# Kernel tuning notes

Hardware: AMD Instinct MI355X
Metric: run time of the kernel (lower is better)

Reference implementation:

```python
import jax, jax.numpy as jnp
import numpy as np

N, D = 1024, 64  # n_nodes, inputSize == hiddenSize == cellSize


def setup_inputs() -> dict:
    key = jax.random.key(0)
    ks = jax.random.split(key, 9)
    inputs = jax.random.normal(ks[0], (N, D), dtype=jnp.float32)
    # sparse-ish binary adjacency, no self loops
    adj = (jax.random.uniform(ks[1], (N, N)) < 0.03).astype(jnp.float32)
    adj = adj.at[jnp.arange(N), jnp.arange(N)].set(0.0)
    numNei = jnp.maximum(adj.sum(axis=1), 1.0)  # avoid div-by-zero
    # initStates() in torch uses randn for h0/c0
    h0 = jax.random.normal(ks[2], (N, D), dtype=jnp.float32)
    c0 = jax.random.normal(ks[3], (N, D), dtype=jnp.float32)
    # torch nn.Linear default init: U(-1/sqrt(fan_in), 1/sqrt(fan_in))
    s_g = 1.0 / np.sqrt(2 * D)
    s_h = 1.0 / np.sqrt(D)
    Wg = jax.random.uniform(ks[4], (D, 2 * D), minval=-s_g, maxval=s_g, dtype=jnp.float32)
    bg = jax.random.uniform(ks[5], (D,), minval=-s_g, maxval=s_g, dtype=jnp.float32)
    Ws = jax.random.uniform(ks[6], (D, D), minval=-s_h, maxval=s_h, dtype=jnp.float32)
    bs = jax.random.uniform(ks[7], (D,), minval=-s_h, maxval=s_h, dtype=jnp.float32)
    Wn = jax.random.uniform(ks[8], (D, D), minval=-s_h, maxval=s_h, dtype=jnp.float32)
    sequence = jnp.arange(N, dtype=jnp.int32)
    return {"inputs": inputs, "neighbour": adj, "numNei": numNei,
            "h0": h0, "c0": c0, "Wg": Wg, "bg": bg, "Ws": Ws, "bs": bs,
            "Wn": Wn, "sequence": sequence}


def reference(inputs, neighbour, numNei, h0, c0, Wg, bg, Ws, bs, Wn, sequence):
    def step(carry, idx):
        H, C = carry                       # [N, D] each
        inp = inputs[idx]                  # [D]
        h_i = H[idx]                       # [D]
        c_i = C[idx]                       # [D] (torch passes cellState[index])
        nei = neighbour[idx]               # [N] adjacency row
        num = numNei[idx]
        # neighbour-averaged hidden state
        neiH = (nei @ H) / num             # [D]
        pre = jnp.concatenate([inp, h_i]) @ Wg.T + bg + neiH @ Wn.T  # [D]
        inputState = jax.nn.sigmoid(pre)
        outputState = inputState           # identical expression in torch
        helpCell = jnp.tanh(pre)
        fs = inp @ Ws.T + bs               # selfGate(inp), [D]
        # forgetSelfMat broadcast of fs over all nodes
        neiForget = jax.nn.sigmoid(fs[None, :] + H @ Wn.T)   # [N, D]
        forgetState = jax.nn.sigmoid(fs + h_i @ Wn.T)        # [D]
        c_new = (nei @ (neiForget * c_i[None, :])) / num \
                + forgetState * c_i + inputState * helpCell  # [D]
        h_new = jnp.tanh(outputState * c_new)
        return (H.at[idx].set(h_new), C.at[idx].set(c_new)), None

    (Hf, _Cf), _ = jax.lax.scan(step, (h0, c0), sequence)
    # torch: residualHidden aliases hiddenState and is mutated in-place,
    # so `hiddenState + residualHidden` == 2 * final hidden state.
    return Hf + Hf
```

## Files before the change

kernel.cpp:

```cpp
#include <hip/hip_runtime.h>

#define NN 1024
#define DD 64
#define CAP 96
#define RCAP 128
#define SENT 32768
#define NL2E -1.44269504088896f

typedef __attribute__((ext_vector_type(8))) short bf16x8;
typedef __attribute__((ext_vector_type(4))) float f32x4;

__device__ uint4    WnFragD[8*64];
__device__ float    FSd[NN*DD];
__device__ float    Gd[NN*DD];
__device__ float    preBaseD[NN*DD];
__device__ float    fpreD[NN*DD];
__device__ float4   nodeDatD[NN*DD];
__device__ int      lowNeiD[NN*CAP + 64];
__device__ int      revNeiD[NN*RCAP];
__device__ int      revCntD[NN];
__device__ int2     hdrD[NN];
__device__ int      posArr[NN];
__device__ float    invNumD[NN];

__device__ __forceinline__ float sigm(float x)  { return 1.0f / (1.0f + __expf(-x)); }
__device__ __forceinline__ float tanhf_(float x){ return 2.0f / (1.0f + __expf(-2.0f*x)) - 1.0f; }
__device__ __forceinline__ unsigned short bf16r(float x) {
  unsigned u = __float_as_uint(x);
  u = u + 0x7fffu + ((u >> 16) & 1u);
  return (unsigned short)(u >> 16);
}

__global__ __launch_bounds__(256) void k_node(const int* __restrict__ seq,
                                              const float* __restrict__ numNei,
                                              const float* __restrict__ inputs,
                                              const float* __restrict__ h0,
                                              const float* __restrict__ Wg,
                                              const float* __restrict__ bg,
                                              const float* __restrict__ Ws,
                                              const float* __restrict__ bs,
                                              const float* __restrict__ Wn) {
  __shared__ float x_l[4][64];
  __shared__ float hh_l[4][64];
  int tid = threadIdx.x;
  int gid = blockIdx.x * 256 + tid;
  if (gid < NN) { posArr[seq[gid]] = gid; invNumD[gid] = 1.0f / numNei[gid]; revCntD[gid] = 0; }
  if (gid < 512) {
    int st = gid >> 6, lane = gid & 63;
    int s = st >> 2, t = st & 3;
    int row = 16*t + (lane & 15);
    int k0 = 32*s + 8*(lane >> 4);
    const float* wr = &Wn[row*64 + k0];
    uint4 f;
    f.x = (unsigned)bf16r(wr[0]) | ((unsigned)bf16r(wr[1]) << 16);
    f.y = (unsigned)bf16r(wr[2]) | ((unsigned)bf16r(wr[3]) << 16);
    f.z = (unsigned)bf16r(wr[4]) | ((unsigned)bf16r(wr[5]) << 16);
    f.w = (unsigned)bf16r(wr[6]) | ((unsigned)bf16r(wr[7]) << 16);
    WnFragD[st*64 + lane] = f;
  }
  for (int e2 = gid; e2 < NN*CAP; e2 += 256*256) lowNeiD[e2] = SENT;
  int w = tid >> 6, d = tid & 63;
  int i = blockIdx.x * 4 + w;
  x_l[w][d]  = inputs[i*DD + d];
  hh_l[w][d] = h0[i*DD + d];
  __syncthreads();
  float afs = bs[d], apre = bg[d], ag0 = 0.0f;
  const float4* wsr = (const float4*)&Ws[d*64];
  const float4* wnr = (const float4*)&Wn[d*64];
  const float4* wga = (const float4*)&Wg[d*128];
  const float4* wgb = (const float4*)&Wg[d*128 + 64];
  #pragma unroll 4
  for (int k4 = 0; k4 < 16; ++k4) {
    float4 ws4 = wsr[k4], wn4 = wnr[k4], wa4 = wga[k4], wb4 = wgb[k4];
    const float* wsp = (const float*)&ws4;
    const float* wnp = (const float*)&wn4;
    const float* wap = (const float*)&wa4;
    const float* wbp = (const float*)&wb4;
    #pragma unroll
    for (int j = 0; j < 4; ++j) {
      int k = 4*k4 + j;
      float xk = x_l[w][k], hk = hh_l[w][k];
      afs  += xk * wsp[j];
      ag0  += hk * wnp[j];
      apre += xk * wap[j] + hk * wbp[j];
    }
  }
  FSd[i*DD + d]      = afs;
  Gd[i*DD + d]       = ag0;
  preBaseD[i*DD + d] = apre;
  fpreD[i*DD + d]    = sigm(afs + ag0);
}

__global__ __launch_bounds__(256) void k_edges(const float* __restrict__ adj,
                                               const float* __restrict__ c0) {
  int tid = threadIdx.x;
  int w = tid >> 6, d = tid & 63;
  int i = blockIdx.x * 4 + w;
  int pi = posArr[i];
  float fs = FSd[i*DD + d];
  float accP = 0.0f, accS = 0.0f;
  int cnt = 0;
  for (int base = 0; base < NN; base += 64) {
    float a = adj[i*NN + base + d];
    unsigned long long mask = __ballot(a != 0.0f);
    while (mask) {
      int b = __ffsll(mask) - 1;
      mask &= (mask - 1);
      int j = base + b;
      if (posArr[j] < pi) {
        if (d == 0 && cnt < 64) {
          lowNeiD[i*CAP + cnt] = j << 5;
          int slot = atomicAdd(&revCntD[j], 1);
          if (slot < RCAP) revNeiD[j*RCAP + slot] = i;
        }
        cnt++;
      } else {
        float g = Gd[j*DD + d];
        accP += g;
        accS += sigm(fs + g);
      }
    }
  }
  float inv = invNumD[i];
  if (d == 0) {
    int ccap = (cnt < 64) ? cnt : 64;
    hdrD[i] = make_int2(ccap, __float_as_int(inv));
  }
  float c0v = c0[i*DD + d];
  float civ = c0v * inv;
  nodeDatD[i*DD + d] = make_float4(NL2E * fs,
                                   preBaseD[i*DD + d] + accP * inv,
                                   civ,
                                   c0v * fpreD[i*DD + d] + civ * accS);
}

__global__ __launch_bounds__(1024, 4) void k_seq(float* __restrict__ out) {
  __shared__ unsigned long long Gl64[(NN*DD + 64)/4];
  __shared__ unsigned low8p[NN][4];
  __shared__ int      queue_[NN];
  __shared__ int      indeg[NN];
  __shared__ float    invL[NN];
  __shared__ unsigned short hstage[16][64];
  __shared__ int head, tail;
  unsigned short* Gl = (unsigned short*)Gl64;
  int tid  = threadIdx.x;
  int lane = tid & 63, w = tid >> 6;
  if (tid == 0) { head = 0; tail = 0; }
  queue_[tid] = -1;
  int2 hdr = hdrD[tid];
  int  rc  = revCntD[tid];
  int  cnt0 = hdr.x;
  indeg[tid] = cnt0 | (cnt0 << 8) | (rc << 15);
  invL[tid]  = __int_as_float(hdr.y);
  {
    uint4 a = *(const uint4*)&lowNeiD[tid*CAP];
    uint4 b = *(const uint4*)&lowNeiD[tid*CAP + 4];
    low8p[tid][0] = (a.x & 0xffffu) | (a.y << 16);
    low8p[tid][1] = (a.z & 0xffffu) | (a.w << 16);
    low8p[tid][2] = (b.x & 0xffffu) | (b.y << 16);
    low8p[tid][3] = (b.z & 0xffffu) | (b.w << 16);
  }
  if (tid < 16) Gl64[NN*DD/4 + tid] = 0ull;
  uint4 fb[2][4];
  #pragma unroll
  for (int s = 0; s < 2; ++s) {
    #pragma unroll
    for (int t = 0; t < 4; ++t)
      fb[s][t] = WnFragD[(s*4 + t)*64 + lane];
  }
  __syncthreads();
  if (cnt0 == 0) {
    int p = __hip_atomic_fetch_add(&tail, 1, __ATOMIC_RELAXED, __HIP_MEMORY_SCOPE_WORKGROUP);
    __hip_atomic_store(&queue_[p], tid | (rc << 17), __ATOMIC_RELEASE, __HIP_MEMORY_SCOPE_WORKGROUP);
  }
  __syncthreads();

  int t0 = 0;
  if (lane == 0) t0 = __hip_atomic_fetch_add(&head, 1, __ATOMIC_RELAXED, __HIP_MEMORY_SCOPE_WORKGROUP);
  int t = __builtin_amdgcn_readfirstlane(t0);
  int e = -1;
  if (t < NN) {
    e = __hip_atomic_load(&queue_[t], __ATOMIC_ACQUIRE, __HIP_MEMORY_SCOPE_WORKGROUP);
    while (e < 0)
      e = __hip_atomic_load(&queue_[t], __ATOMIC_ACQUIRE, __HIP_MEMORY_SCOPE_WORKGROUP);
  } else {
    return;
  }
  e = __builtin_amdgcn_readfirstlane(e);

  int    i, cnt, rcnt, jb2v, r0, r1;
  float4 nd;
  float  inv;
  uint4  lvv;
  #define ISSUE(E) do {                                               \
    i    = (E) & 1023;                                                \
    cnt  = ((E) >> 10) & 127;                                         \
    rcnt = ((E) >> 17) & 255;                                         \
    nd   = nodeDatD[i*DD + lane];                                     \
    jb2v = lowNeiD[i*CAP + 8 + lane];                                 \
    r0   = (lane < rcnt)      ? revNeiD[i*RCAP + lane]      : -1;     \
    r1   = (lane + 64 < rcnt) ? revNeiD[i*RCAP + 64 + lane] : -1;     \
    inv  = invL[i];                                                   \
    lvv  = *(uint4*)&low8p[i][0];                                     \
  } while (0)
  ISSUE(e);

  float4 tA0 = {0,0,0,0}, tA1 = {0,0,0,0};
  int    tB0 = 0, tB1 = 0;

  for (;;) {
    asm volatile("" :: "v"(tA0.x), "v"(tA0.y), "v"(tA0.z), "v"(tA0.w),
                       "v"(tA1.x), "v"(tA1.y), "v"(tA1.z), "v"(tA1.w),
                       "v"(tB0), "v"(tB1));
    float fs2n = nd.x;
    float accG = 0.0f, accS = 0.0f;
    float g0[8], g1[8], g2[8], g3[8];
    #define LD(c) __uint_as_float(((unsigned)Gl[((c) << 1) + lane]) << 16)
    if (cnt > 0) {
      unsigned v0=lvv.x&0xffffu, v1=lvv.x>>16, v2=lvv.y&0xffffu, v3=lvv.y>>16;
      unsigned v4=lvv.z&0xffffu, v5=lvv.z>>16, v6=lvv.w&0xffffu, v7=lvv.w>>16;
      g0[0]=LD(v0); g0[1]=LD(v1); g0[2]=LD(v2); g0[3]=LD(v3);
      g0[4]=LD(v4); g0[5]=LD(v5); g0[6]=LD(v6); g0[7]=LD(v7);
    }
    if (cnt > 8) {
      #pragma unroll
      for (int q = 0; q < 8; ++q) g1[q] = LD(__builtin_amdgcn_readlane(jb2v, q));
    }
    if (cnt > 16) {
      #pragma unroll
      for (int q = 0; q < 8; ++q) g2[q] = LD(__builtin_amdgcn_readlane(jb2v, 8 + q));
    }
    if (cnt > 24) {
      #pragma unroll
      for (int q = 0; q < 8; ++q) g3[q] = LD(__builtin_amdgcn_readlane(jb2v, 16 + q));
    }
    auto domath = [&](float G) {
      float x_ = __builtin_fmaf(G, NL2E, fs2n);
      float e_ = __builtin_amdgcn_exp2f(x_);
      accS += __builtin_amdgcn_rcpf(1.0f + e_);
      accG += G;
    };
    if (cnt > 0) {
      #pragma unroll
      for (int q = 0; q < 8; ++q) domath(g0[q]);
    }
    if (cnt > 8) {
      #pragma unroll
      for (int q = 0; q < 8; ++q) domath(g1[q]);
    }
    if (cnt > 16) {
      #pragma unroll
      for (int q = 0; q < 8; ++q) domath(g2[q]);
    }
    if (cnt > 24) {
      #pragma unroll
      for (int q = 0; q < 8; ++q) domath(g3[q]);
    }
    if (cnt > 32) {
      for (int base = 32; base < cnt; base += 8) {
        float gg[8];
        #pragma unroll
        for (int q = 0; q < 8; ++q) gg[q] = LD(__builtin_amdgcn_readlane(jb2v, base - 8 + q));
        #pragma unroll
        for (int q = 0; q < 8; ++q) domath(gg[q]);
      }
    }
    {
      int nb8 = (cnt + 7) & ~7;
      float sig0 = __builtin_amdgcn_rcpf(1.0f + __builtin_amdgcn_exp2f(fs2n));
      accS -= (float)(nb8 - cnt) * sig0;
    }
    float pre = nd.y + inv * accG;
    float is  = sigm(pre);
    float hcl = tanhf_(pre);
    float c   = nd.z * accS + nd.w + is * hcl;
    float h   = tanhf_(is * c);
    int ic = i, r0c = r0, r1c = r1;
    if (lane == 0) t0 = __hip_atomic_fetch_add(&head, 1, __ATOMIC_RELAXED, __HIP_MEMORY_SCOPE_WORKGROUP);
    t = __builtin_amdgcn_readfirstlane(t0);
    bool done = (t >= NN);
    int e2 = -1;
    if (!done) e2 = __hip_atomic_load(&queue_[t], __ATOMIC_ACQUIRE, __HIP_MEMORY_SCOPE_WORKGROUP);
    e2 = __builtin_amdgcn_readfirstlane(e2);
    bool pre_ok = (e2 >= 0);
    if (pre_ok) ISSUE(e2);
    hstage[w][lane] = bf16r(h);
    const uint4* hv = (const uint4*)&hstage[w][0];
    uint4 fa0 = hv[lane >> 4];
    uint4 fa1 = hv[4 + (lane >> 4)];
    f32x4 z = {0.f, 0.f, 0.f, 0.f};
    f32x4 a0 = __builtin_amdgcn_mfma_f32_16x16x32_bf16(__builtin_bit_cast(bf16x8, fa0), __builtin_bit_cast(bf16x8, fb[0][0]), z, 0, 0, 0);
    f32x4 a1 = __builtin_amdgcn_mfma_f32_16x16x32_bf16(__builtin_bit_cast(bf16x8, fa0), __builtin_bit_cast(bf16x8, fb[0][1]), z, 0, 0, 0);
    f32x4 a2 = __builtin_amdgcn_mfma_f32_16x16x32_bf16(__builtin_bit_cast(bf16x8, fa0), __builtin_bit_cast(bf16x8, fb[0][2]), z, 0, 0, 0);
    f32x4 a3 = __builtin_amdgcn_mfma_f32_16x16x32_bf16(__builtin_bit_cast(bf16x8, fa0), __builtin_bit_cast(bf16x8, fb[0][3]), z, 0, 0, 0);
    a0 = __builtin_amdgcn_mfma_f32_16x16x32_bf16(__builtin_bit_cast(bf16x8, fa1), __builtin_bit_cast(bf16x8, fb[1][0]), a0, 0, 0, 0);
    a1 = __builtin_amdgcn_mfma_f32_16x16x32_bf16(__builtin_bit_cast(bf16x8, fa1), __builtin_bit_cast(bf16x8, fb[1][1]), a1, 0, 0, 0);
    a2 = __builtin_amdgcn_mfma_f32_16x16x32_bf16(__builtin_bit_cast(bf16x8, fa1), __builtin_bit_cast(bf16x8, fb[1][2]), a2, 0, 0, 0);
    a3 = __builtin_amdgcn_mfma_f32_16x16x32_bf16(__builtin_bit_cast(bf16x8, fa1), __builtin_bit_cast(bf16x8, fb[1][3]), a3, 0, 0, 0);
    float r01 = (lane & 16) ? a1[0] : a0[0];
    float r23 = (lane & 16) ? a3[0] : a2[0];
    float rg  = (lane & 32) ? r23 : r01;
    Gl[(ic << 6) + lane] = bf16r(rg);
    int push0 = -1, push1 = -1;
    if (r0c >= 0) {
      int old = __hip_atomic_fetch_add(&indeg[r0c], -1, __ATOMIC_ACQ_REL, __HIP_MEMORY_SCOPE_WORKGROUP);
      if ((old & 0xff) == 1) {
        int p = __hip_atomic_fetch_add(&tail, 1, __ATOMIC_RELAXED, __HIP_MEMORY_SCOPE_WORKGROUP);
        int en = r0c | (((old >> 8) & 127) << 10) | (((old >> 15) & 255) << 17);
        __hip_atomic_store(&queue_[p], en, __ATOMIC_RELEASE, __HIP_MEMORY_SCOPE_WORKGROUP);
        push0 = r0c;
      }
    }
    if (r1c >= 0) {
      int old = __hip_atomic_fetch_add(&indeg[r1c], -1, __ATOMIC_ACQ_REL, __HIP_MEMORY_SCOPE_WORKGROUP);
      if ((old & 0xff) == 1) {
        int p = __hip_atomic_fetch_add(&tail, 1, __ATOMIC_RELAXED, __HIP_MEMORY_SCOPE_WORKGROUP);
        int en = r1c | (((old >> 8) & 127) << 10) | (((old >> 15) & 255) << 17);
        __hip_atomic_store(&queue_[p], en, __ATOMIC_RELEASE, __HIP_MEMORY_SCOPE_WORKGROUP);
        push1 = r1c;
      }
    }
    {
      unsigned long long pm0 = __ballot(push0 >= 0);
      unsigned long long pm1 = __ballot(push1 >= 0);
      int rdA = -1, rdB = -1;
      if (pm0) {
        int b = __ffsll(pm0) - 1;
        rdA = __builtin_amdgcn_readlane(push0, b);
        pm0 &= (pm0 - 1);
      }
      if (pm0) {
        int b = __ffsll(pm0) - 1;
        rdB = __builtin_amdgcn_readlane(push0, b);
      } else if (pm1) {
        int b = __ffsll(pm1) - 1;
        rdB = __builtin_amdgcn_readlane(push1, b);
      }
      if (rdA >= 0) {
        tA0 = nodeDatD[rdA*DD + lane];
        tB0 = lowNeiD[rdA*CAP + 8 + lane];
      }
      if (rdB >= 0) {
        tA1 = nodeDatD[rdB*DD + lane];
        tB1 = lowNeiD[rdB*CAP + 8 + lane];
      }
    }
    out[ic*DD + lane] = 2.0f * h;
    if (done) break;
    if (!pre_ok) {
      int e3 = __hip_atomic_load(&queue_[t], __ATOMIC_ACQUIRE, __HIP_MEMORY_SCOPE_WORKGROUP);
      while (e3 < 0)
        e3 = __hip_atomic_load(&queue_[t], __ATOMIC_ACQUIRE, __HIP_MEMORY_SCOPE_WORKGROUP);
      e3 = __builtin_amdgcn_readfirstlane(e3);
      ISSUE(e3);
    }
  }
  #undef LD
  #undef ISSUE
}

extern "C" void kernel_launch(void* const* d_in, const int* in_sizes, int n_in,
                              void* d_out, int out_size, void* d_ws, size_t ws_size,
                              hipStream_t stream) {
  const float* inputs = (const float*)d_in[0];
  const float* adj    = (const float*)d_in[1];
  const float* numNei = (const float*)d_in[2];
  const float* h0     = (const float*)d_in[3];
  const float* c0     = (const float*)d_in[4];
  const float* Wg     = (const float*)d_in[5];
  const float* bg     = (const float*)d_in[6];
  const float* Ws     = (const float*)d_in[7];
  const float* bs     = (const float*)d_in[8];
  const float* Wn     = (const float*)d_in[9];
  const int*   seq    = (const int*)d_in[10];
  float* out = (float*)d_out;

  k_node <<<256, 256, 0, stream>>>(seq, numNei, inputs, h0, Wg, bg, Ws, bs, Wn);
  k_edges<<<256, 256, 0, stream>>>(adj, c0);
  k_seq  <<<1, 1024, 0, stream>>>(out);
}
```

Before: 216.6 us.

## Switch sequential dependency gather to push-based global atomic accumulation

The sequential kernel previously gathered each node's lower-order neighbours' G values from a large bf16 shared-memory cache when processing it. Now each finished node pushes its G value and the per-target sigmoid term directly into global accumulators (accGd/accSd) for all reverse neighbours with atomicAdd, and consumers just load the accumulated sums. This removes the shared G cache and the neighbour lists, reducing LDS footprint and per-node gather work. In exchange it adds global float atomics and a vmcnt wait on the serial critical path, plus fp32 storage instead of bf16 for the accumulated G.

```diff
diff --git a/kernel.cpp b/kernel.cpp
--- a/kernel.cpp
+++ b/kernel.cpp
@@ -2,26 +2,26 @@
 
 #define NN 1024
 #define DD 64
-#define CAP 96
 #define RCAP 128
-#define SENT 32768
 #define NL2E -1.44269504088896f
 
 typedef __attribute__((ext_vector_type(8))) short bf16x8;
 typedef __attribute__((ext_vector_type(4))) float f32x4;
 
-__device__ uint4    WnFragD[8*64];
-__device__ float    FSd[NN*DD];
-__device__ float    Gd[NN*DD];
-__device__ float    preBaseD[NN*DD];
-__device__ float    fpreD[NN*DD];
-__device__ float4   nodeDatD[NN*DD];
-__device__ int      lowNeiD[NN*CAP + 64];
-__device__ int      revNeiD[NN*RCAP];
-__device__ int      revCntD[NN];
-__device__ int2     hdrD[NN];
-__device__ int      posArr[NN];
-__device__ float    invNumD[NN];
+__device__ uint4  WnFragD[8*64];
+__device__ float  FSd[NN*DD];
+__device__ float  Gd[NN*DD];
+__device__ float  preBaseD[NN*DD];
+__device__ float  fpreD[NN*DD];
+__device__ float4 nodeDatD[NN*DD];
+__device__ float  fs2nD[(NN+1)*DD];
+__device__ float  accGd[(NN+1)*DD];
+__device__ float  accSd[(NN+1)*DD];
+__device__ int    revNeiD[NN*RCAP];
+__device__ int    revCntD[NN];
+__device__ int    cntD[NN];
+__device__ int    posArr[NN];
+__device__ float  invNumD[NN];
 
 __device__ __forceinline__ float sigm(float x)  { return 1.0f / (1.0f + __expf(-x)); }
 __device__ __forceinline__ float tanhf_(float x){ return 2.0f / (1.0f + __expf(-2.0f*x)) - 1.0f; }
@@ -58,7 +58,8 @@
     f.w = (unsigned)bf16r(wr[6]) | ((unsigned)bf16r(wr[7]) << 16);
     WnFragD[st*64 + lane] = f;
   }
-  for (int e2 = gid; e2 < NN*CAP; e2 += 256*256) lowNeiD[e2] = SENT;
+  for (int e2 = gid; e2 < NN*RCAP; e2 += 256*256) revNeiD[e2] = NN;
+  if (gid < DD) { fs2nD[NN*DD + gid] = 0.0f; accGd[NN*DD + gid] = 0.0f; accSd[NN*DD + gid] = 0.0f; }
   int w = tid >> 6, d = tid & 63;
   int i = blockIdx.x * 4 + w;
   x_l[w][d]  = inputs[i*DD + d];
@@ -108,8 +109,7 @@
       mask &= (mask - 1);
       int j = base + b;
       if (posArr[j] < pi) {
-        if (d == 0 && cnt < 64) {
-          lowNeiD[i*CAP + cnt] = j << 5;
+        if (d == 0) {
           int slot = atomicAdd(&revCntD[j], 1);
           if (slot < RCAP) revNeiD[j*RCAP + slot] = i;
         }
@@ -122,45 +122,30 @@
     }
   }
   float inv = invNumD[i];
-  if (d == 0) {
-    int ccap = (cnt < 64) ? cnt : 64;
-    hdrD[i] = make_int2(ccap, __float_as_int(inv));
-  }
+  if (d == 0) cntD[i] = cnt;
   float c0v = c0[i*DD + d];
   float civ = c0v * inv;
-  nodeDatD[i*DD + d] = make_float4(NL2E * fs,
+  nodeDatD[i*DD + d] = make_float4(inv,
                                    preBaseD[i*DD + d] + accP * inv,
                                    civ,
                                    c0v * fpreD[i*DD + d] + civ * accS);
+  fs2nD[i*DD + d] = NL2E * fs;
+  accGd[i*DD + d] = 0.0f;
+  accSd[i*DD + d] = 0.0f;
 }
 
 __global__ __launch_bounds__(1024, 4) void k_seq(float* __restrict__ out) {
-  __shared__ unsigned long long Gl64[(NN*DD + 64)/4];
-  __shared__ unsigned low8p[NN][4];
-  __shared__ int      queue_[NN];
-  __shared__ int      indeg[NN];
-  __shared__ float    invL[NN];
+  __shared__ int queue_[NN];
+  __shared__ int indeg[NN];
   __shared__ unsigned short hstage[16][64];
   __shared__ int head, tail;
-  unsigned short* Gl = (unsigned short*)Gl64;
   int tid  = threadIdx.x;
   int lane = tid & 63, w = tid >> 6;
   if (tid == 0) { head = 0; tail = 0; }
   queue_[tid] = -1;
-  int2 hdr = hdrD[tid];
-  int  rc  = revCntD[tid];
-  int  cnt0 = hdr.x;
-  indeg[tid] = cnt0 | (cnt0 << 8) | (rc << 15);
-  invL[tid]  = __int_as_float(hdr.y);
-  {
-    uint4 a = *(const uint4*)&lowNeiD[tid*CAP];
-    uint4 b = *(const uint4*)&lowNeiD[tid*CAP + 4];
-    low8p[tid][0] = (a.x & 0xffffu) | (a.y << 16);
-    low8p[tid][1] = (a.z & 0xffffu) | (a.w << 16);
-    low8p[tid][2] = (b.x & 0xffffu) | (b.y << 16);
-    low8p[tid][3] = (b.z & 0xffffu) | (b.w << 16);
-  }
-  if (tid < 16) Gl64[NN*DD/4 + tid] = 0ull;
+  int cnt0 = cntD[tid];
+  int rc   = revCntD[tid]; if (rc > 255) rc = 255;
+  indeg[tid] = cnt0 | (rc << 15);
   uint4 fb[2][4];
   #pragma unroll
   for (int s = 0; s < 2; ++s) {
@@ -188,94 +173,27 @@
   }
   e = __builtin_amdgcn_readfirstlane(e);
 
-  int    i, cnt, rcnt, jb2v, r0, r1;
+  int    i, rcnt, r0v, r1v;
   float4 nd;
-  float  inv;
-  uint4  lvv;
-  #define ISSUE(E) do {                                               \
-    i    = (E) & 1023;                                                \
-    cnt  = ((E) >> 10) & 127;                                         \
-    rcnt = ((E) >> 17) & 255;                                         \
-    nd   = nodeDatD[i*DD + lane];                                     \
-    jb2v = lowNeiD[i*CAP + 8 + lane];                                 \
-    r0   = (lane < rcnt)      ? revNeiD[i*RCAP + lane]      : -1;     \
-    r1   = (lane + 64 < rcnt) ? revNeiD[i*RCAP + 64 + lane] : -1;     \
-    inv  = invL[i];                                                   \
-    lvv  = *(uint4*)&low8p[i][0];                                     \
+  float  aG, aS;
+  #define ISSUE(E) do {                                                          \
+    i    = (E) & 1023;                                                           \
+    rcnt = ((E) >> 17) & 255;                                                    \
+    nd   = nodeDatD[i*DD + lane];                                                \
+    aG   = __hip_atomic_load(&accGd[i*DD + lane], __ATOMIC_RELAXED, __HIP_MEMORY_SCOPE_AGENT); \
+    aS   = __hip_atomic_load(&accSd[i*DD + lane], __ATOMIC_RELAXED, __HIP_MEMORY_SCOPE_AGENT); \
+    r0v  = revNeiD[i*RCAP + lane];                                               \
+    r1v  = revNeiD[i*RCAP + 64 + lane];                                          \
   } while (0)
   ISSUE(e);
 
-  float4 tA0 = {0,0,0,0}, tA1 = {0,0,0,0};
-  int    tB0 = 0, tB1 = 0;
-
   for (;;) {
-    asm volatile("" :: "v"(tA0.x), "v"(tA0.y), "v"(tA0.z), "v"(tA0.w),
-                       "v"(tA1.x), "v"(tA1.y), "v"(tA1.z), "v"(tA1.w),
-                       "v"(tB0), "v"(tB1));
-    float fs2n = nd.x;
-    float accG = 0.0f, accS = 0.0f;
-    float g0[8], g1[8], g2[8], g3[8];
-    #define LD(c) __uint_as_float(((unsigned)Gl[((c) << 1) + lane]) << 16)
-    if (cnt > 0) {
-      unsigned v0=lvv.x&0xffffu, v1=lvv.x>>16, v2=lvv.y&0xffffu, v3=lvv.y>>16;
-      unsigned v4=lvv.z&0xffffu, v5=lvv.z>>16, v6=lvv.w&0xffffu, v7=lvv.w>>16;
-      g0[0]=LD(v0); g0[1]=LD(v1); g0[2]=LD(v2); g0[3]=LD(v3);
-      g0[4]=LD(v4); g0[5]=LD(v5); g0[6]=LD(v6); g0[7]=LD(v7);
-    }
-    if (cnt > 8) {
-      #pragma unroll
-      for (int q = 0; q < 8; ++q) g1[q] = LD(__builtin_amdgcn_readlane(jb2v, q));
-    }
-    if (cnt > 16) {
-      #pragma unroll
-      for (int q = 0; q < 8; ++q) g2[q] = LD(__builtin_amdgcn_readlane(jb2v, 8 + q));
-    }
-    if (cnt > 24) {
-      #pragma unroll
-      for (int q = 0; q < 8; ++q) g3[q] = LD(__builtin_amdgcn_readlane(jb2v, 16 + q));
-    }
-    auto domath = [&](float G) {
-      float x_ = __builtin_fmaf(G, NL2E, fs2n);
-      float e_ = __builtin_amdgcn_exp2f(x_);
-      accS += __builtin_amdgcn_rcpf(1.0f + e_);
-      accG += G;
-    };
-    if (cnt > 0) {
-      #pragma unroll
-      for (int q = 0; q < 8; ++q) domath(g0[q]);
-    }
-    if (cnt > 8) {
-      #pragma unroll
-      for (int q = 0; q < 8; ++q) domath(g1[q]);
-    }
-    if (cnt > 16) {
-      #pragma unroll
-      for (int q = 0; q < 8; ++q) domath(g2[q]);
-    }
-    if (cnt > 24) {
-      #pragma unroll
-      for (int q = 0; q < 8; ++q) domath(g3[q]);
-    }
-    if (cnt > 32) {
-      for (int base = 32; base < cnt; base += 8) {
-        float gg[8];
-        #pragma unroll
-        for (int q = 0; q < 8; ++q) gg[q] = LD(__builtin_amdgcn_readlane(jb2v, base - 8 + q));
-        #pragma unroll
-        for (int q = 0; q < 8; ++q) domath(gg[q]);
-      }
-    }
-    {
-      int nb8 = (cnt + 7) & ~7;
-      float sig0 = __builtin_amdgcn_rcpf(1.0f + __builtin_amdgcn_exp2f(fs2n));
-      accS -= (float)(nb8 - cnt) * sig0;
-    }
-    float pre = nd.y + inv * accG;
+    float pre = nd.y + nd.x * aG;
     float is  = sigm(pre);
     float hcl = tanhf_(pre);
-    float c   = nd.z * accS + nd.w + is * hcl;
+    float c   = nd.z * aS + nd.w + is * hcl;
     float h   = tanhf_(is * c);
-    int ic = i, r0c = r0, r1c = r1;
+    int ic = i, rcur = rcnt, rv0 = r0v, rv1 = r1v;
     if (lane == 0) t0 = __hip_atomic_fetch_add(&head, 1, __ATOMIC_RELAXED, __HIP_MEMORY_SCOPE_WORKGROUP);
     t = __builtin_amdgcn_readfirstlane(t0);
     bool done = (t >= NN);
@@ -300,49 +218,43 @@
     float r01 = (lane & 16) ? a1[0] : a0[0];
     float r23 = (lane & 16) ? a3[0] : a2[0];
     float rg  = (lane & 32) ? r23 : r01;
-    Gl[(ic << 6) + lane] = bf16r(rg);
-    int push0 = -1, push1 = -1;
-    if (r0c >= 0) {
-      int old = __hip_atomic_fetch_add(&indeg[r0c], -1, __ATOMIC_ACQ_REL, __HIP_MEMORY_SCOPE_WORKGROUP);
+    for (int base = 0; base < rcur; base += 8) {
+      int   ids[8];
+      float fsd[8];
+      #pragma unroll
+      for (int q = 0; q < 8; ++q) {
+        int idx = base + q;
+        int id  = (idx < 64) ? __builtin_amdgcn_readlane(rv0, idx)
+                             : __builtin_amdgcn_readlane(rv1, idx - 64);
+        id = (idx < rcur) ? id : NN;
+        ids[q] = id;
+        fsd[q] = fs2nD[id*DD + lane];
+      }
+      float sv[8];
+      #pragma unroll
+      for (int q = 0; q < 8; ++q) {
+        float x_ = __builtin_fmaf(rg, NL2E, fsd[q]);
+        sv[q] = __builtin_amdgcn_rcpf(1.0f + __builtin_amdgcn_exp2f(x_));
+      }
+      #pragma unroll
+      for (int q = 0; q < 8; ++q) {
+        atomicAdd(&accSd[ids[q]*DD + lane], sv[q]);
+        atomicAdd(&accGd[ids[q]*DD + lane], rg);
+      }
+    }
+    asm volatile("s_waitcnt vmcnt(0)" ::: "memory");
+    if (lane < rcur) {
+      int old = __hip_atomic_fetch_add(&indeg[rv0], -1, __ATOMIC_ACQ_REL, __HIP_MEMORY_SCOPE_WORKGROUP);
       if ((old & 0xff) == 1) {
         int p = __hip_atomic_fetch_add(&tail, 1, __ATOMIC_RELAXED, __HIP_MEMORY_SCOPE_WORKGROUP);
-        int en = r0c | (((old >> 8) & 127) << 10) | (((old >> 15) & 255) << 17);
-        __hip_atomic_store(&queue_[p], en, __ATOMIC_RELEASE, __HIP_MEMORY_SCOPE_WORKGROUP);
-        push0 = r0c;
-      }
-    }
-    if (r1c >= 0) {
-      int old = __hip_atomic_fetch_add(&indeg[r1c], -1, __ATOMIC_ACQ_REL, __HIP_MEMORY_SCOPE_WORKGROUP);
+        __hip_atomic_store(&queue_[p], rv0 | (((old >> 15) & 255) << 17), __ATOMIC_RELEASE, __HIP_MEMORY_SCOPE_WORKGROUP);
+      }
+    }
+    if (lane + 64 < rcur) {
+      int old = __hip_atomic_fetch_add(&indeg[rv1], -1, __ATOMIC_ACQ_REL, __HIP_MEMORY_SCOPE_WORKGROUP);
       if ((old & 0xff) == 1) {
         int p = __hip_atomic_fetch_add(&tail, 1, __ATOMIC_RELAXED, __HIP_MEMORY_SCOPE_WORKGROUP);
-        int en = r1c | (((old >> 8) & 127) << 10) | (((old >> 15) & 255) << 17);
-        __hip_atomic_store(&queue_[p], en, __ATOMIC_RELEASE, __HIP_MEMORY_SCOPE_WORKGROUP);
-        push1 = r1c;
-      }
-    }
-    {
-      unsigned long long pm0 = __ballot(push0 >= 0);
-      unsigned long long pm1 = __ballot(push1 >= 0);
-      int rdA = -1, rdB = -1;
-      if (pm0) {
-        int b = __ffsll(pm0) - 1;
-        rdA = __builtin_amdgcn_readlane(push0, b);
-        pm0 &= (pm0 - 1);
-      }
-      if (pm0) {
-        int b = __ffsll(pm0) - 1;
-        rdB = __builtin_amdgcn_readlane(push0, b);
-      } else if (pm1) {
-        int b = __ffsll(pm1) - 1;
-        rdB = __builtin_amdgcn_readlane(push1, b);
-      }
-      if (rdA >= 0) {
-        tA0 = nodeDatD[rdA*DD + lane];
-        tB0 = lowNeiD[rdA*CAP + 8 + lane];
-      }
-      if (rdB >= 0) {
-        tA1 = nodeDatD[rdB*DD + lane];
-        tB1 = lowNeiD[rdB*CAP + 8 + lane];
+        __hip_atomic_store(&queue_[p], rv1 | (((old >> 15) & 255) << 17), __ATOMIC_RELEASE, __HIP_MEMORY_SCOPE_WORKGROUP);
       }
     }
     out[ic*DD + lane] = 2.0f * h;
@@ -355,7 +267,6 @@
       ISSUE(e3);
     }
   }
-  #undef LD
   #undef ISSUE
 }
 
```

Result: slower. 434.3 us (+100.5%).

## Combine four sigmoids per reciprocal and drop speculative prefetch of pushed nodes

Applied to the files above, without the earlier changes.

Neighbour gathers are regrouped into chunks of four, and each chunk's four sigmoid terms are summed over a shared denominator, so one reciprocal serves four neighbours instead of one each. Exponent inputs are clamped to avoid overflow in the product of denominators. Padding correction now works at 4-slot instead of 8-slot granularity. The ballot, readlane and cache-warming loads of newly ready nodes are removed, trimming per-step overhead on the serial critical path at the risk of colder loads later.

```diff
diff --git a/kernel.cpp b/kernel.cpp
--- a/kernel.cpp
+++ b/kernel.cpp
@@ -205,70 +205,83 @@
   } while (0)
   ISSUE(e);
 
-  float4 tA0 = {0,0,0,0}, tA1 = {0,0,0,0};
-  int    tB0 = 0, tB1 = 0;
-
   for (;;) {
-    asm volatile("" :: "v"(tA0.x), "v"(tA0.y), "v"(tA0.z), "v"(tA0.w),
-                       "v"(tA1.x), "v"(tA1.y), "v"(tA1.z), "v"(tA1.w),
-                       "v"(tB0), "v"(tB1));
     float fs2n = nd.x;
     float accG = 0.0f, accS = 0.0f;
-    float g0[8], g1[8], g2[8], g3[8];
+    float g[32];
     #define LD(c) __uint_as_float(((unsigned)Gl[((c) << 1) + lane]) << 16)
     if (cnt > 0) {
-      unsigned v0=lvv.x&0xffffu, v1=lvv.x>>16, v2=lvv.y&0xffffu, v3=lvv.y>>16;
-      unsigned v4=lvv.z&0xffffu, v5=lvv.z>>16, v6=lvv.w&0xffffu, v7=lvv.w>>16;
-      g0[0]=LD(v0); g0[1]=LD(v1); g0[2]=LD(v2); g0[3]=LD(v3);
-      g0[4]=LD(v4); g0[5]=LD(v5); g0[6]=LD(v6); g0[7]=LD(v7);
+      g[0]=LD(lvv.x & 0xffffu); g[1]=LD(lvv.x >> 16);
+      g[2]=LD(lvv.y & 0xffffu); g[3]=LD(lvv.y >> 16);
+    }
+    if (cnt > 4) {
+      g[4]=LD(lvv.z & 0xffffu); g[5]=LD(lvv.z >> 16);
+      g[6]=LD(lvv.w & 0xffffu); g[7]=LD(lvv.w >> 16);
     }
     if (cnt > 8) {
       #pragma unroll
-      for (int q = 0; q < 8; ++q) g1[q] = LD(__builtin_amdgcn_readlane(jb2v, q));
+      for (int q = 0; q < 4; ++q) g[8+q]  = LD(__builtin_amdgcn_readlane(jb2v, q));
+    }
+    if (cnt > 12) {
+      #pragma unroll
+      for (int q = 0; q < 4; ++q) g[12+q] = LD(__builtin_amdgcn_readlane(jb2v, 4+q));
     }
     if (cnt > 16) {
       #pragma unroll
-      for (int q = 0; q < 8; ++q) g2[q] = LD(__builtin_amdgcn_readlane(jb2v, 8 + q));
+      for (int q = 0; q < 4; ++q) g[16+q] = LD(__builtin_amdgcn_readlane(jb2v, 8+q));
+    }
+    if (cnt > 20) {
+      #pragma unroll
+      for (int q = 0; q < 4; ++q) g[20+q] = LD(__builtin_amdgcn_readlane(jb2v, 12+q));
     }
     if (cnt > 24) {
       #pragma unroll
-      for (int q = 0; q < 8; ++q) g3[q] = LD(__builtin_amdgcn_readlane(jb2v, 16 + q));
-    }
-    auto domath = [&](float G) {
-      float x_ = __builtin_fmaf(G, NL2E, fs2n);
-      float e_ = __builtin_amdgcn_exp2f(x_);
-      accS += __builtin_amdgcn_rcpf(1.0f + e_);
-      accG += G;
+      for (int q = 0; q < 4; ++q) g[24+q] = LD(__builtin_amdgcn_readlane(jb2v, 16+q));
+    }
+    if (cnt > 28) {
+      #pragma unroll
+      for (int q = 0; q < 4; ++q) g[28+q] = LD(__builtin_amdgcn_readlane(jb2v, 20+q));
+    }
+    auto quad = [&](float ga, float gb, float gc, float gd) {
+      float xa = fminf(__builtin_fmaf(ga, NL2E, fs2n), 25.0f);
+      float xb = fminf(__builtin_fmaf(gb, NL2E, fs2n), 25.0f);
+      float xc = fminf(__builtin_fmaf(gc, NL2E, fs2n), 25.0f);
+      float xd = fminf(__builtin_fmaf(gd, NL2E, fs2n), 25.0f);
+      float ea = __builtin_amdgcn_exp2f(xa);
+      float eb = __builtin_amdgcn_exp2f(xb);
+      float ec = __builtin_amdgcn_exp2f(xc);
+      float ed = __builtin_amdgcn_exp2f(xd);
+      float s0 = ea + eb, n0 = s0 + 2.0f;
+      float d0 = __builtin_fmaf(ea, eb, s0) + 1.0f;
+      float s1 = ec + ed, n1 = s1 + 2.0f;
+      float d1 = __builtin_fmaf(ec, ed, s1) + 1.0f;
+      float Nn = __builtin_fmaf(n0, d1, n1 * d0);
+      float Dd = d0 * d1;
+      accS = __builtin_fmaf(Nn, __builtin_amdgcn_rcpf(Dd), accS);
+      accG += (ga + gb) + (gc + gd);
     };
-    if (cnt > 0) {
-      #pragma unroll
-      for (int q = 0; q < 8; ++q) domath(g0[q]);
-    }
-    if (cnt > 8) {
-      #pragma unroll
-      for (int q = 0; q < 8; ++q) domath(g1[q]);
-    }
-    if (cnt > 16) {
-      #pragma unroll
-      for (int q = 0; q < 8; ++q) domath(g2[q]);
-    }
-    if (cnt > 24) {
-      #pragma unroll
-      for (int q = 0; q < 8; ++q) domath(g3[q]);
-    }
+    if (cnt > 0)  quad(g[0],  g[1],  g[2],  g[3]);
+    if (cnt > 4)  quad(g[4],  g[5],  g[6],  g[7]);
+    if (cnt > 8)  quad(g[8],  g[9],  g[10], g[11]);
+    if (cnt > 12) quad(g[12], g[13], g[14], g[15]);
+    if (cnt > 16) quad(g[16], g[17], g[18], g[19]);
+    if (cnt > 20) quad(g[20], g[21], g[22], g[23]);
+    if (cnt > 24) quad(g[24], g[25], g[26], g[27]);
+    if (cnt > 28) quad(g[28], g[29], g[30], g[31]);
     if (cnt > 32) {
-      for (int base = 32; base < cnt; base += 8) {
-        float gg[8];
-        #pragma unroll
-        for (int q = 0; q < 8; ++q) gg[q] = LD(__builtin_amdgcn_readlane(jb2v, base - 8 + q));
-        #pragma unroll
-        for (int q = 0; q < 8; ++q) domath(gg[q]);
+      for (int base = 32; base < cnt; base += 4) {
+        float ga = LD(__builtin_amdgcn_readlane(jb2v, base - 8));
+        float gb = LD(__builtin_amdgcn_readlane(jb2v, base - 7));
+        float gc = LD(__builtin_amdgcn_readlane(jb2v, base - 6));
+        float gd = LD(__builtin_amdgcn_readlane(jb2v, base - 5));
+        quad(ga, gb, gc, gd);
       }
     }
     {
-      int nb8 = (cnt + 7) & ~7;
-      float sig0 = __builtin_amdgcn_rcpf(1.0f + __builtin_amdgcn_exp2f(fs2n));
-      accS -= (float)(nb8 - cnt) * sig0;
+      int slots = (cnt <= 32) ? ((cnt + 3) & ~3) : (32 + ((cnt - 32 + 3) & ~3));
+      float e0   = __builtin_amdgcn_exp2f(fminf(fs2n, 25.0f));
+      float sig0 = __builtin_amdgcn_rcpf(1.0f + e0);
+      accS -= (float)(slots - cnt) * sig0;
     }
     float pre = nd.y + inv * accG;
     float is  = sigm(pre);
@@ -301,14 +314,12 @@
     float r23 = (lane & 16) ? a3[0] : a2[0];
     float rg  = (lane & 32) ? r23 : r01;
     Gl[(ic << 6) + lane] = bf16r(rg);
-    int push0 = -1, push1 = -1;
     if (r0c >= 0) {
       int old = __hip_atomic_fetch_add(&indeg[r0c], -1, __ATOMIC_ACQ_REL, __HIP_MEMORY_SCOPE_WORKGROUP);
       if ((old & 0xff) == 1) {
         int p = __hip_atomic_fetch_add(&tail, 1, __ATOMIC_RELAXED, __HIP_MEMORY_SCOPE_WORKGROUP);
         int en = r0c | (((old >> 8) & 127) << 10) | (((old >> 15) & 255) << 17);
         __hip_atomic_store(&queue_[p], en, __ATOMIC_RELEASE, __HIP_MEMORY_SCOPE_WORKGROUP);
-        push0 = r0c;
       }
     }
     if (r1c >= 0) {
@@ -317,32 +328,6 @@
         int p = __hip_atomic_fetch_add(&tail, 1, __ATOMIC_RELAXED, __HIP_MEMORY_SCOPE_WORKGROUP);
         int en = r1c | (((old >> 8) & 127) << 10) | (((old >> 15) & 255) << 17);
         __hip_atomic_store(&queue_[p], en, __ATOMIC_RELEASE, __HIP_MEMORY_SCOPE_WORKGROUP);
-        push1 = r1c;
-      }
-    }
-    {
-      unsigned long long pm0 = __ballot(push0 >= 0);
-      unsigned long long pm1 = __ballot(push1 >= 0);
-      int rdA = -1, rdB = -1;
-      if (pm0) {
-        int b = __ffsll(pm0) - 1;
-        rdA = __builtin_amdgcn_readlane(push0, b);
-        pm0 &= (pm0 - 1);
-      }
-      if (pm0) {
-        int b = __ffsll(pm0) - 1;
-        rdB = __builtin_amdgcn_readlane(push0, b);
-      } else if (pm1) {
-        int b = __ffsll(pm1) - 1;
-        rdB = __builtin_amdgcn_readlane(push1, b);
-      }
-      if (rdA >= 0) {
-        tA0 = nodeDatD[rdA*DD + lane];
-        tB0 = lowNeiD[rdA*CAP + 8 + lane];
-      }
-      if (rdB >= 0) {
-        tA1 = nodeDatD[rdB*DD + lane];
-        tB1 = lowNeiD[rdB*CAP + 8 + lane];
       }
     }
     out[ic*DD + lane] = 2.0f * h;
```

After: 209.0 us. -3.5%, faster.

## Spread sequential dependency scheduling across multiple blocks with NaN-flagged global publish

Applied to the files above, without the earlier changes.

Replaces the single-workgroup dynamic topological queue in LDS with a static round-robin assignment of sequence positions to waves across 8 blocks. Each wave spins on global memory, where unpublished G rows are marked with a NaN sentinel, until all lower-ordered neighbour G values are available, then publishes its own G row with agent-scope atomics. This drops the reverse-neighbour lists, in-degree counters and queue bookkeeping, and spreads work over more CUs. In exchange, neighbour reads go through L2 instead of LDS, G is kept in fp32 instead of bf16, and waves busy-poll, so a static ordering can stall behind slow predecessors.

```diff
diff --git a/kernel.cpp b/kernel.cpp
--- a/kernel.cpp
+++ b/kernel.cpp
@@ -3,9 +3,10 @@
 #define NN 1024
 #define DD 64
 #define CAP 96
-#define RCAP 128
 #define SENT 32768
 #define NL2E -1.44269504088896f
+#define NBLK 8
+#define NWAVE (NBLK*16)
 
 typedef __attribute__((ext_vector_type(8))) short bf16x8;
 typedef __attribute__((ext_vector_type(4))) float f32x4;
@@ -16,9 +17,8 @@
 __device__ float    preBaseD[NN*DD];
 __device__ float    fpreD[NN*DD];
 __device__ float4   nodeDatD[NN*DD];
+__device__ float    GpubD[(NN+1)*DD];
 __device__ int      lowNeiD[NN*CAP + 64];
-__device__ int      revNeiD[NN*RCAP];
-__device__ int      revCntD[NN];
 __device__ int2     hdrD[NN];
 __device__ int      posArr[NN];
 __device__ float    invNumD[NN];
@@ -44,7 +44,7 @@
   __shared__ float hh_l[4][64];
   int tid = threadIdx.x;
   int gid = blockIdx.x * 256 + tid;
-  if (gid < NN) { posArr[seq[gid]] = gid; invNumD[gid] = 1.0f / numNei[gid]; revCntD[gid] = 0; }
+  if (gid < NN) { posArr[seq[gid]] = gid; invNumD[gid] = 1.0f / numNei[gid]; }
   if (gid < 512) {
     int st = gid >> 6, lane = gid & 63;
     int s = st >> 2, t = st & 3;
@@ -58,6 +58,7 @@
     f.w = (unsigned)bf16r(wr[6]) | ((unsigned)bf16r(wr[7]) << 16);
     WnFragD[st*64 + lane] = f;
   }
+  if (gid < DD) GpubD[NN*DD + gid] = 0.0f;
   for (int e2 = gid; e2 < NN*CAP; e2 += 256*256) lowNeiD[e2] = SENT;
   int w = tid >> 6, d = tid & 63;
   int i = blockIdx.x * 4 + w;
@@ -98,6 +99,7 @@
   int i = blockIdx.x * 4 + w;
   int pi = posArr[i];
   float fs = FSd[i*DD + d];
+  GpubD[i*DD + d] = __int_as_float(0x7FC00000);
   float accP = 0.0f, accS = 0.0f;
   int cnt = 0;
   for (int base = 0; base < NN; base += 64) {
@@ -108,11 +110,7 @@
       mask &= (mask - 1);
       int j = base + b;
       if (posArr[j] < pi) {
-        if (d == 0 && cnt < 64) {
-          lowNeiD[i*CAP + cnt] = j << 5;
-          int slot = atomicAdd(&revCntD[j], 1);
-          if (slot < RCAP) revNeiD[j*RCAP + slot] = i;
-        }
+        if (d == 0 && cnt < 64) lowNeiD[i*CAP + cnt] = j << 5;
         cnt++;
       } else {
         float g = Gd[j*DD + d];
@@ -134,33 +132,12 @@
                                    c0v * fpreD[i*DD + d] + civ * accS);
 }
 
-__global__ __launch_bounds__(1024, 4) void k_seq(float* __restrict__ out) {
-  __shared__ unsigned long long Gl64[(NN*DD + 64)/4];
-  __shared__ unsigned low8p[NN][4];
-  __shared__ int      queue_[NN];
-  __shared__ int      indeg[NN];
-  __shared__ float    invL[NN];
+__global__ __launch_bounds__(1024, 4) void k_seq(const int* __restrict__ seq,
+                                                 float* __restrict__ out) {
   __shared__ unsigned short hstage[16][64];
-  __shared__ int head, tail;
-  unsigned short* Gl = (unsigned short*)Gl64;
   int tid  = threadIdx.x;
   int lane = tid & 63, w = tid >> 6;
-  if (tid == 0) { head = 0; tail = 0; }
-  queue_[tid] = -1;
-  int2 hdr = hdrD[tid];
-  int  rc  = revCntD[tid];
-  int  cnt0 = hdr.x;
-  indeg[tid] = cnt0 | (cnt0 << 8) | (rc << 15);
-  invL[tid]  = __int_as_float(hdr.y);
-  {
-    uint4 a = *(const uint4*)&lowNeiD[tid*CAP];
-    uint4 b = *(const uint4*)&lowNeiD[tid*CAP + 4];
-    low8p[tid][0] = (a.x & 0xffffu) | (a.y << 16);
-    low8p[tid][1] = (a.z & 0xffffu) | (a.w << 16);
-    low8p[tid][2] = (b.x & 0xffffu) | (b.y << 16);
-    low8p[tid][3] = (b.z & 0xffffu) | (b.w << 16);
-  }
-  if (tid < 16) Gl64[NN*DD/4 + tid] = 0ull;
+  int wid  = blockIdx.x * 16 + w;
   uint4 fb[2][4];
   #pragma unroll
   for (int s = 0; s < 2; ++s) {
@@ -168,122 +145,94 @@
     for (int t = 0; t < 4; ++t)
       fb[s][t] = WnFragD[(s*4 + t)*64 + lane];
   }
-  __syncthreads();
-  if (cnt0 == 0) {
-    int p = __hip_atomic_fetch_add(&tail, 1, __ATOMIC_RELAXED, __HIP_MEMORY_SCOPE_WORKGROUP);
-    __hip_atomic_store(&queue_[p], tid | (rc << 17), __ATOMIC_RELEASE, __HIP_MEMORY_SCOPE_WORKGROUP);
-  }
-  __syncthreads();
-
-  int t0 = 0;
-  if (lane == 0) t0 = __hip_atomic_fetch_add(&head, 1, __ATOMIC_RELAXED, __HIP_MEMORY_SCOPE_WORKGROUP);
-  int t = __builtin_amdgcn_readfirstlane(t0);
-  int e = -1;
-  if (t < NN) {
-    e = __hip_atomic_load(&queue_[t], __ATOMIC_ACQUIRE, __HIP_MEMORY_SCOPE_WORKGROUP);
-    while (e < 0)
-      e = __hip_atomic_load(&queue_[t], __ATOMIC_ACQUIRE, __HIP_MEMORY_SCOPE_WORKGROUP);
-  } else {
-    return;
-  }
-  e = __builtin_amdgcn_readfirstlane(e);
-
-  int    i, cnt, rcnt, jb2v, r0, r1;
-  float4 nd;
-  float  inv;
-  uint4  lvv;
-  #define ISSUE(E) do {                                               \
-    i    = (E) & 1023;                                                \
-    cnt  = ((E) >> 10) & 127;                                         \
-    rcnt = ((E) >> 17) & 255;                                         \
-    nd   = nodeDatD[i*DD + lane];                                     \
-    jb2v = lowNeiD[i*CAP + 8 + lane];                                 \
-    r0   = (lane < rcnt)      ? revNeiD[i*RCAP + lane]      : -1;     \
-    r1   = (lane + 64 < rcnt) ? revNeiD[i*RCAP + 64 + lane] : -1;     \
-    inv  = invL[i];                                                   \
-    lvv  = *(uint4*)&low8p[i][0];                                     \
-  } while (0)
-  ISSUE(e);
-
-  float4 tA0 = {0,0,0,0}, tA1 = {0,0,0,0};
-  int    tB0 = 0, tB1 = 0;
+
+  int p = wid;
+  int i = seq[p];
+  int2 hd = hdrD[i];
+  float4 nd = nodeDatD[i*DD + lane];
+  int jbv = lowNeiD[i*CAP + lane];
+  int cnt = hd.x;
+  float inv = __int_as_float(hd.y);
+
+  #define ALD(c) __hip_atomic_load(&GpubD[((c) << 1) + lane], __ATOMIC_RELAXED, __HIP_MEMORY_SCOPE_AGENT)
 
   for (;;) {
-    asm volatile("" :: "v"(tA0.x), "v"(tA0.y), "v"(tA0.z), "v"(tA0.w),
-                       "v"(tA1.x), "v"(tA1.y), "v"(tA1.z), "v"(tA1.w),
-                       "v"(tB0), "v"(tB1));
+    int pn = p + NWAVE;
+    bool more = (pn < NN);
+    int i2 = 0, cnt2 = 0, jbv2 = 0;
+    float inv2 = 0.0f;
+    float4 nd2 = {0.f, 0.f, 0.f, 0.f};
+    if (more) {
+      i2 = seq[pn];
+      int2 hd2 = hdrD[i2];
+      nd2  = nodeDatD[i2*DD + lane];
+      jbv2 = lowNeiD[i2*CAP + lane];
+      cnt2 = hd2.x;
+      inv2 = __int_as_float(hd2.y);
+    }
     float fs2n = nd.x;
-    float accG = 0.0f, accS = 0.0f;
-    float g0[8], g1[8], g2[8], g3[8];
-    #define LD(c) __uint_as_float(((unsigned)Gl[((c) << 1) + lane]) << 16)
-    if (cnt > 0) {
-      unsigned v0=lvv.x&0xffffu, v1=lvv.x>>16, v2=lvv.y&0xffffu, v3=lvv.y>>16;
-      unsigned v4=lvv.z&0xffffu, v5=lvv.z>>16, v6=lvv.w&0xffffu, v7=lvv.w>>16;
-      g0[0]=LD(v0); g0[1]=LD(v1); g0[2]=LD(v2); g0[3]=LD(v3);
-      g0[4]=LD(v4); g0[5]=LD(v5); g0[6]=LD(v6); g0[7]=LD(v7);
-    }
-    if (cnt > 8) {
-      #pragma unroll
-      for (int q = 0; q < 8; ++q) g1[q] = LD(__builtin_amdgcn_readlane(jb2v, q));
-    }
-    if (cnt > 16) {
-      #pragma unroll
-      for (int q = 0; q < 8; ++q) g2[q] = LD(__builtin_amdgcn_readlane(jb2v, 8 + q));
-    }
-    if (cnt > 24) {
-      #pragma unroll
-      for (int q = 0; q < 8; ++q) g3[q] = LD(__builtin_amdgcn_readlane(jb2v, 16 + q));
-    }
-    auto domath = [&](float G) {
-      float x_ = __builtin_fmaf(G, NL2E, fs2n);
-      float e_ = __builtin_amdgcn_exp2f(x_);
-      accS += __builtin_amdgcn_rcpf(1.0f + e_);
-      accG += G;
-    };
-    if (cnt > 0) {
-      #pragma unroll
-      for (int q = 0; q < 8; ++q) domath(g0[q]);
-    }
-    if (cnt > 8) {
-      #pragma unroll
-      for (int q = 0; q < 8; ++q) domath(g1[q]);
-    }
-    if (cnt > 16) {
-      #pragma unroll
-      for (int q = 0; q < 8; ++q) domath(g2[q]);
-    }
-    if (cnt > 24) {
-      #pragma unroll
-      for (int q = 0; q < 8; ++q) domath(g3[q]);
-    }
-    if (cnt > 32) {
-      for (int base = 32; base < cnt; base += 8) {
-        float gg[8];
-        #pragma unroll
-        for (int q = 0; q < 8; ++q) gg[q] = LD(__builtin_amdgcn_readlane(jb2v, base - 8 + q));
-        #pragma unroll
-        for (int q = 0; q < 8; ++q) domath(gg[q]);
-      }
-    }
+    float accG, accS;
+    do {
+      accG = 0.0f; accS = 0.0f;
+      float g0[8], g1[8], g2[8], g3[8];
+      if (cnt > 0) {
+        #pragma unroll
+        for (int q = 0; q < 8; ++q) g0[q] = ALD(__builtin_amdgcn_readlane(jbv, q));
+      }
+      if (cnt > 8) {
+        #pragma unroll
+        for (int q = 0; q < 8; ++q) g1[q] = ALD(__builtin_amdgcn_readlane(jbv, 8 + q));
+      }
+      if (cnt > 16) {
+        #pragma unroll
+        for (int q = 0; q < 8; ++q) g2[q] = ALD(__builtin_amdgcn_readlane(jbv, 16 + q));
+      }
+      if (cnt > 24) {
+        #pragma unroll
+        for (int q = 0; q < 8; ++q) g3[q] = ALD(__builtin_amdgcn_readlane(jbv, 24 + q));
+      }
+      auto domath = [&](float G) {
+        float x_ = __builtin_fmaf(G, NL2E, fs2n);
+        float e_ = __builtin_amdgcn_exp2f(x_);
+        accS += __builtin_amdgcn_rcpf(1.0f + e_);
+        accG += G;
+      };
+      if (cnt > 0) {
+        #pragma unroll
+        for (int q = 0; q < 8; ++q) domath(g0[q]);
+      }
+      if (cnt > 8) {
+        #pragma unroll
+        for (int q = 0; q < 8; ++q) domath(g1[q]);
+      }
+      if (cnt > 16) {
+        #pragma unroll
+        for (int q = 0; q < 8; ++q) domath(g2[q]);
+      }
+      if (cnt > 24) {
+        #pragma unroll
+        for (int q = 0; q < 8; ++q) domath(g3[q]);
+      }
+      if (cnt > 32) {
+        for (int base = 32; base < cnt; base += 8) {
+          float gg[8];
+          #pragma unroll
+          for (int q = 0; q < 8; ++q) gg[q] = ALD(__builtin_amdgcn_readlane(jbv, base + q));
+          #pragma unroll
+          for (int q = 0; q < 8; ++q) domath(gg[q]);
+        }
+      }
+    } while (__any((accG != accG) || (accS != accS)));
     {
-      int nb8 = (cnt + 7) & ~7;
+      int npad = (8 - (cnt & 7)) & 7;
       float sig0 = __builtin_amdgcn_rcpf(1.0f + __builtin_amdgcn_exp2f(fs2n));
-      accS -= (float)(nb8 - cnt) * sig0;
+      accS -= (float)npad * sig0;
     }
     float pre = nd.y + inv * accG;
     float is  = sigm(pre);
     float hcl = tanhf_(pre);
     float c   = nd.z * accS + nd.w + is * hcl;
     float h   = tanhf_(is * c);
-    int ic = i, r0c = r0, r1c = r1;
-    if (lane == 0) t0 = __hip_atomic_fetch_add(&head, 1, __ATOMIC_RELAXED, __HIP_MEMORY_SCOPE_WORKGROUP);
-    t = __builtin_amdgcn_readfirstlane(t0);
-    bool done = (t >= NN);
-    int e2 = -1;
-    if (!done) e2 = __hip_atomic_load(&queue_[t], __ATOMIC_ACQUIRE, __HIP_MEMORY_SCOPE_WORKGROUP);
-    e2 = __builtin_amdgcn_readfirstlane(e2);
-    bool pre_ok = (e2 >= 0);
-    if (pre_ok) ISSUE(e2);
     hstage[w][lane] = bf16r(h);
     const uint4* hv = (const uint4*)&hstage[w][0];
     uint4 fa0 = hv[lane >> 4];
@@ -300,63 +249,12 @@
     float r01 = (lane & 16) ? a1[0] : a0[0];
     float r23 = (lane & 16) ? a3[0] : a2[0];
     float rg  = (lane & 32) ? r23 : r01;
-    Gl[(ic << 6) + lane] = bf16r(rg);
-    int push0 = -1, push1 = -1;
-    if (r0c >= 0) {
-      int old = __hip_atomic_fetch_add(&indeg[r0c], -1, __ATOMIC_ACQ_REL, __HIP_MEMORY_SCOPE_WORKGROUP);
-      if ((old & 0xff) == 1) {
-        int p = __hip_atomic_fetch_add(&tail, 1, __ATOMIC_RELAXED, __HIP_MEMORY_SCOPE_WORKGROUP);
-        int en = r0c | (((old >> 8) & 127) << 10) | (((old >> 15) & 255) << 17);
-        __hip_atomic_store(&queue_[p], en, __ATOMIC_RELEASE, __HIP_MEMORY_SCOPE_WORKGROUP);
-        push0 = r0c;
-      }
-    }
-    if (r1c >= 0) {
-      int old = __hip_atomic_fetch_add(&indeg[r1c], -1, __ATOMIC_ACQ_REL, __HIP_MEMORY_SCOPE_WORKGROUP);
-      if ((old & 0xff) == 1) {
-        int p = __hip_atomic_fetch_add(&tail, 1, __ATOMIC_RELAXED, __HIP_MEMORY_SCOPE_WORKGROUP);
-        int en = r1c | (((old >> 8) & 127) << 10) | (((old >> 15) & 255) << 17);
-        __hip_atomic_store(&queue_[p], en, __ATOMIC_RELEASE, __HIP_MEMORY_SCOPE_WORKGROUP);
-        push1 = r1c;
-      }
-    }
-    {
-      unsigned long long pm0 = __ballot(push0 >= 0);
-      unsigned long long pm1 = __ballot(push1 >= 0);
-      int rdA = -1, rdB = -1;
-      if (pm0) {
-        int b = __ffsll(pm0) - 1;
-        rdA = __builtin_amdgcn_readlane(push0, b);
-        pm0 &= (pm0 - 1);
-      }
-      if (pm0) {
-        int b = __ffsll(pm0) - 1;
-        rdB = __builtin_amdgcn_readlane(push0, b);
-      } else if (pm1) {
-        int b = __ffsll(pm1) - 1;
-        rdB = __builtin_amdgcn_readlane(push1, b);
-      }
-      if (rdA >= 0) {
-        tA0 = nodeDatD[rdA*DD + lane];
-        tB0 = lowNeiD[rdA*CAP + 8 + lane];
-      }
-      if (rdB >= 0) {
-        tA1 = nodeDatD[rdB*DD + lane];
-        tB1 = lowNeiD[rdB*CAP + 8 + lane];
-      }
-    }
-    out[ic*DD + lane] = 2.0f * h;
-    if (done) break;
-    if (!pre_ok) {
-      int e3 = __hip_atomic_load(&queue_[t], __ATOMIC_ACQUIRE, __HIP_MEMORY_SCOPE_WORKGROUP);
-      while (e3 < 0)
-        e3 = __hip_atomic_load(&queue_[t], __ATOMIC_ACQUIRE, __HIP_MEMORY_SCOPE_WORKGROUP);
-      e3 = __builtin_amdgcn_readfirstlane(e3);
-      ISSUE(e3);
-    }
-  }
-  #undef LD
-  #undef ISSUE
+    __hip_atomic_store(&GpubD[(i << 6) + lane], rg, __ATOMIC_RELAXED, __HIP_MEMORY_SCOPE_AGENT);
+    out[i*DD + lane] = 2.0f * h;
+    if (!more) break;
+    p = pn; i = i2; cnt = cnt2; inv = inv2; nd = nd2; jbv = jbv2;
+  }
+  #undef ALD
 }
 
 extern "C" void kernel_launch(void* const* d_in, const int* in_sizes, int n_in,
@@ -377,5 +275,5 @@
 
   k_node <<<256, 256, 0, stream>>>(seq, numNei, inputs, h0, Wg, bg, Ws, bs, Wn);
   k_edges<<<256, 256, 0, stream>>>(adj, c0);
-  k_seq  <<<1, 1024, 0, stream>>>(out);
-}
+  k_seq  <<<NBLK, 1024, 0, stream>>>(seq, out);
+}
```

Measured after the change: 201.8 us. 1.07x faster.
